# Kernel tuning notes

Measured on AMD Instinct MI355X. Metric: run time of the kernel, lower is better.

Reference implementation:

```python
import jax, jax.numpy as jnp
import numpy as np

TOPK = 8
MIN_TEMP = 0.5
NEG = -1e9  # finite stand-in for -inf (same softmax result, safe grads)


def setup_inputs() -> dict:
    key = jax.random.key(0)
    ks = jax.random.split(key, 6)
    B, S, D, N, K = 4, 4096, 1024, 256, 8
    token_states = jax.random.normal(ks[0], (B, S, D), dtype=jnp.float32)
    set_states = jax.random.normal(ks[1], (B, N, D), dtype=jnp.float32)
    desc_router = jax.random.normal(ks[2], (N, D), dtype=jnp.float32)
    token_to_sets = jax.random.randint(ks[3], (S, K), 0, N)
    Wq = jax.random.normal(ks[4], (D, D), dtype=jnp.float32) / np.sqrt(D)
    bq = jnp.zeros((D,), dtype=jnp.float32)
    temperature = jnp.ones((1,), dtype=jnp.float32)
    return {"token_states": token_states, "set_states": set_states,
            "desc_router": desc_router, "token_to_sets": token_to_sets,
            "Wq": Wq, "bq": bq, "temperature": temperature}


def reference(token_states, set_states, desc_router, token_to_sets, Wq, bq, temperature):
    B, S, D = token_states.shape
    N = set_states.shape[1]
    scale = 1.0 / np.sqrt(D)

    # q = Linear(token_states)
    q = jnp.einsum('bsd,ed->bse', token_states, Wq) + bq
    scores = jnp.einsum('bse,ne->bsn', q, desc_router) * scale  # [B,S,N]

    # restrict_to_sets: boolean routing mask built by scatter
    rows = jnp.broadcast_to(jnp.arange(S)[:, None], token_to_sets.shape)
    cols = jnp.clip(token_to_sets, 0, N - 1)
    valid = token_to_sets >= 0
    mask = jnp.zeros((S, N), dtype=bool).at[rows, cols].max(valid)
    scores = jnp.where(mask[None], scores, NEG)

    # top-k keep (topk < num_sets)
    topk_scores, topk_idx = jax.lax.top_k(scores, TOPK)
    b_idx = jnp.arange(B)[:, None, None]
    s_idx = jnp.arange(S)[None, :, None]
    keep = jnp.full_like(scores, NEG).at[b_idx, s_idx, topk_idx].set(topk_scores)

    temp = jnp.maximum(temperature, MIN_TEMP)  # clamp(min=0.5)
    weights = jax.nn.softmax(keep / temp, axis=-1)  # [B,S,N]
    token_repr = jnp.einsum('bsn,bnd->bsd', weights, set_states)
    bank_indices = jnp.argmax(weights, axis=-1)
    return token_repr, bank_indices, weights, topk_idx
```

## Files before the change

### kernel.cpp

```cpp
#include <hip/hip_runtime.h>
#include <math.h>
#include <float.h>


namespace {
constexpr int kB = 4, kS = 4096, kD = 1024, kN = 256, kK = 8;
constexpr float kScale = 0.03125f;
constexpr float kNeg = -1e9f;
constexpr float kLog2e = 1.4426950408889634f;
constexpr size_t kBankOff = (size_t)kB * kS * kD;
constexpr size_t kWOff    = kBankOff + (size_t)kB * kS;
constexpr size_t kTopkOff = kWOff + (size_t)kB * kS * kN;
constexpr int kEC = 8;
constexpr int kEL = kD / kEC;
constexpr int kNT = kN / 8;
}

#if __has_builtin(__builtin_amdgcn_exp2f)
#define FAST_EXP2(x) __builtin_amdgcn_exp2f(x)
#else
#define FAST_EXP2(x) exp2f(x)
#endif
#if __has_builtin(__builtin_amdgcn_rcpf)
#define FAST_RCP(x) __builtin_amdgcn_rcpf(x)
#else
#define FAST_RCP(x) (1.0f / (x))
#endif

__global__ __launch_bounds__(256) void k_prep(const float* __restrict__ dr,
                                              const float* __restrict__ wq,
                                              float* __restrict__ part) {
  const int nt = blockIdx.x, ec = blockIdx.y, t = threadIdx.x;
  const float4* wq4 = reinterpret_cast<const float4*>(wq);
  float4 acc[8];
#pragma unroll
  for (int j = 0; j < 8; ++j) acc[j] = make_float4(0.f, 0.f, 0.f, 0.f);
  const int e0 = ec * kEL;
#pragma unroll 4
  for (int e = e0; e < e0 + kEL; ++e) {
    const float4 wv = wq4[(size_t)e * (kD / 4) + t];
#pragma unroll
    for (int j = 0; j < 8; ++j) {
      const float a = dr[(size_t)(nt * 8 + j) * kD + e];
      acc[j].x += a * wv.x; acc[j].y += a * wv.y;
      acc[j].z += a * wv.z; acc[j].w += a * wv.w;
    }
  }
  float4* p4 = reinterpret_cast<float4*>(part);
#pragma unroll
  for (int j = 0; j < 8; ++j)
    p4[((size_t)ec * kN + nt * 8 + j) * (kD / 4) + t] = acc[j];
}

__global__ __launch_bounds__(256) void k_reduce(const float* __restrict__ part,
                                                const float* __restrict__ dr,
                                                const float* __restrict__ bq,
                                                float* __restrict__ R,
                                                float* __restrict__ bias) {
  const int n = blockIdx.x, t = threadIdx.x;
  const float4* p4 = reinterpret_cast<const float4*>(part);
  float4 a = make_float4(0.f, 0.f, 0.f, 0.f);
#pragma unroll
  for (int ec = 0; ec < kEC; ++ec) {
    const float4 p = p4[((size_t)ec * kN + n) * (kD / 4) + t];
    a.x += p.x; a.y += p.y; a.z += p.z; a.w += p.w;
  }
  a.x *= kScale; a.y *= kScale; a.z *= kScale; a.w *= kScale;
  reinterpret_cast<float4*>(R)[(size_t)n * (kD / 4) + t] = a;

  if (t < 64) {
    const float4* b4 = reinterpret_cast<const float4*>(bq);
    const float4* dr4 = reinterpret_cast<const float4*>(dr + (size_t)n * kD);
    float p = 0.f;
#pragma unroll
    for (int i = 0; i < 4; ++i) {
      const float4 bb = b4[t * 4 + i];
      const float4 dd = dr4[t * 4 + i];
      p += bb.x * dd.x + bb.y * dd.y + bb.z * dd.z + bb.w * dd.w;
    }
#pragma unroll
    for (int off = 32; off; off >>= 1) p += __shfl_xor(p, off);
    if (t == 0) bias[n] = p * kScale;
  }
}

__global__ __launch_bounds__(256, 4) void k_score(const float* __restrict__ ts,
                                                  const int* __restrict__ t2s,
                                                  const float* __restrict__ R,
                                                  const float* __restrict__ bias,
                                                  const float* __restrict__ temp_p,
                                                  int* __restrict__ st,
                                                  float* __restrict__ out) {
  const int lane = threadIdx.x & 63;
  const int wid = threadIdx.x >> 6;
  const int u = lane & 15;
  const int g = lane >> 4;
  const int s = __builtin_amdgcn_readfirstlane(blockIdx.x * 4 + wid);

  int nraw[kK], nk[kK];
#pragma unroll
  for (int k = 0; k < kK; ++k) {
    nraw[k] = t2s[s * kK + k];
    const int n = nraw[k];
    nk[k] = n < 0 ? 0 : (n > kN - 1 ? kN - 1 : n);
  }
  int validmask = 0;
#pragma unroll
  for (int k = 0; k < kK; ++k) {
    bool v = (nraw[k] >= 0);
#pragma unroll
    for (int j = 0; j < kK; ++j)
      if (j < k && nk[j] == nk[k]) v = false;
    validmask |= v ? (1 << k) : 0;
  }
  const int cnt = __popc(validmask);

  const float4* ts4 = reinterpret_cast<const float4*>(ts);
  const float4* R4 = reinterpret_cast<const float4*>(R);
  const size_t tbase = ((size_t)g * kS + s) * (kD / 4) + u;
  float acc[kK];
#pragma unroll
  for (int k = 0; k < kK; ++k) acc[k] = 0.f;
#pragma unroll 2
  for (int i = 0; i < 16; ++i) {
    const float4 tv = ts4[tbase + i * 16];
#pragma unroll
    for (int k = 0; k < kK; ++k) {
      const float4 rv = R4[(size_t)nk[k] * (kD / 4) + i * 16 + u];
      acc[k] += tv.x * rv.x + tv.y * rv.y + tv.z * rv.z + tv.w * rv.w;
    }
  }

  float pk[kK];
#pragma unroll
  for (int k = 0; k < kK; ++k) {
    float a = acc[k];
    a += __shfl_xor(a, 1);
    a += __shfl_xor(a, 2);
    a += __shfl_xor(a, 4);
    a += __shfl_xor(a, 8);
    pk[k] = a + bias[nk[k]];
  }

  unsigned long long pm0 = 0, pm1 = 0, pm2 = 0, pm3 = 0;
#pragma unroll
  for (int k = 0; k < kK; ++k) {
    const bool v = (validmask >> k) & 1;
    const unsigned long long bit = 1ull << (nk[k] & 63);
    const int wd = nk[k] >> 6;
    pm0 |= (v && wd == 0) ? bit : 0ull;
    pm1 |= (v && wd == 1) ? bit : 0ull;
    pm2 |= (v && wd == 2) ? bit : 0ull;
    pm3 |= (v && wd == 3) ? bit : 0ull;
  }
  int seq[kK];
#pragma unroll
  for (int i = 0; i < kK; ++i) {
    const unsigned long long i0 = ~pm0, i1 = ~pm1, i2 = ~pm2, i3 = ~pm3;
    const int c = i0 ? (__ffsll(i0) - 1)
                     : (i1 ? 64 + (__ffsll(i1) - 1)
                           : (i2 ? 128 + (__ffsll(i2) - 1)
                                 : 192 + (__ffsll(i3) - 1)));
    seq[i] = c;
    const unsigned long long b2 = 1ull << (c & 63);
    const int wd = c >> 6;
    pm0 |= (wd == 0) ? b2 : 0ull;
    pm1 |= (wd == 1) ? b2 : 0ull;
    pm2 |= (wd == 2) ? b2 : 0ull;
    pm3 |= (wd == 3) ? b2 : 0ull;
  }

  float fs[kK];
  int fi[kK];
#pragma unroll
  for (int k = 0; k < kK; ++k) {
    const bool v = (validmask >> k) & 1;
    const int jk = __popc((~validmask) & ((1 << k) - 1));
    int fv = seq[0];
#pragma unroll
    for (int j = 1; j < kK; ++j) fv = (jk == j) ? seq[j] : fv;
    fs[k] = v ? pk[k] : kNeg;
    fi[k] = v ? nk[k] : fv;
  }
#define CE(A, B)                                                        \
  {                                                                     \
    const bool sw = (fs[B] > fs[A]) || (fs[B] == fs[A] && fi[B] < fi[A]); \
    const float fa = fs[A], fb = fs[B];                                 \
    const int ia = fi[A], ib = fi[B];                                   \
    fs[A] = sw ? fb : fa; fs[B] = sw ? fa : fb;                         \
    fi[A] = sw ? ib : ia; fi[B] = sw ? ia : ib;                         \
  }
  CE(0,1) CE(2,3) CE(4,5) CE(6,7)
  CE(0,2) CE(1,3) CE(4,6) CE(5,7)
  CE(1,2) CE(5,6)
  CE(0,4) CE(1,5) CE(2,6) CE(3,7)
  CE(2,4) CE(3,5)
  CE(1,2) CE(3,4) CE(5,6)
#undef CE

  const float it = kLog2e * FAST_RCP(fmaxf(temp_p[0], 0.5f));
  float w[kK];
  float denom = 0.f;
#pragma unroll
  for (int i = 0; i < kK; ++i) {
    const float e = (i < cnt) ? FAST_EXP2((fs[i] - fs[0]) * it) : 0.f;
    w[i] = e;
    denom += e;
  }
  const float rd = FAST_RCP(denom);
#pragma unroll
  for (int i = 0; i < kK; ++i) w[i] *= rd;

  const size_t row = (size_t)g * kS + s;
  if (u < kK) {
    int v = fi[0];
#pragma unroll
    for (int k = 1; k < kK; ++k) v = (u == k) ? fi[k] : v;
    out[kTopkOff + row * kK + u] = (float)v;
  }
  if (u == 0) out[kBankOff + row] = (float)fi[0];

  int sel = 0;
#pragma unroll
  for (int k = 0; k < kK; ++k) {
    sel = (u == k) ? __float_as_int(w[k]) : sel;
    sel = (u == k + kK) ? fi[k] : sel;
  }
  st[row * 16 + u] = sel;
}

__global__ __launch_bounds__(256) void k_repr(const float* __restrict__ ss,
                                              const int* __restrict__ st,
                                              float* __restrict__ out) {
  const int lane = threadIdx.x & 63;
  const int wid = threadIdx.x >> 6;
  const int bid = blockIdx.x;
  const int xcd = bid & 7;
  const int b = xcd >> 1;
  int s_ = ((bid >> 3) << 2) + wid + ((xcd & 1) << 11);
  const int s = __builtin_amdgcn_readfirstlane(s_);
  const size_t row = (size_t)b * kS + s;

  float w[kK];
  int fi[kK];
#pragma unroll
  for (int k = 0; k < kK; ++k) {
    w[k] = __int_as_float(st[row * 16 + k]);
    fi[k] = st[row * 16 + kK + k];
  }

  const float4* ssb = reinterpret_cast<const float4*>(ss) + (size_t)b * kN * (kD / 4);
  float4* o4 = reinterpret_cast<float4*>(out) + row * (kD / 4);
#pragma unroll
  for (int c = 0; c < 4; ++c) {
    float4 v0 = ssb[(size_t)fi[0] * (kD / 4) + c * 64 + lane];
    float4 v1 = ssb[(size_t)fi[1] * (kD / 4) + c * 64 + lane];
    float4 v2 = ssb[(size_t)fi[2] * (kD / 4) + c * 64 + lane];
    float4 v3 = ssb[(size_t)fi[3] * (kD / 4) + c * 64 + lane];
    float4 v4 = ssb[(size_t)fi[4] * (kD / 4) + c * 64 + lane];
    float4 v5 = ssb[(size_t)fi[5] * (kD / 4) + c * 64 + lane];
    float4 v6 = ssb[(size_t)fi[6] * (kD / 4) + c * 64 + lane];
    float4 v7 = ssb[(size_t)fi[7] * (kD / 4) + c * 64 + lane];
    float4 acc;
    acc.x = w[0] * v0.x + w[1] * v1.x + w[2] * v2.x + w[3] * v3.x
          + w[4] * v4.x + w[5] * v5.x + w[6] * v6.x + w[7] * v7.x;
    acc.y = w[0] * v0.y + w[1] * v1.y + w[2] * v2.y + w[3] * v3.y
          + w[4] * v4.y + w[5] * v5.y + w[6] * v6.y + w[7] * v7.y;
    acc.z = w[0] * v0.z + w[1] * v1.z + w[2] * v2.z + w[3] * v3.z
          + w[4] * v4.z + w[5] * v5.z + w[6] * v6.z + w[7] * v7.z;
    acc.w = w[0] * v0.w + w[1] * v1.w + w[2] * v2.w + w[3] * v3.w
          + w[4] * v4.w + w[5] * v5.w + w[6] * v6.w + w[7] * v7.w;
    o4[c * 64 + lane] = acc;
  }

  {
    const int cb = lane * 4;
    float4 wv = make_float4(0.f, 0.f, 0.f, 0.f);
#pragma unroll
    for (int k = 0; k < kK; ++k) {
      wv.x = (fi[k] == cb    ) ? w[k] : wv.x;
      wv.y = (fi[k] == cb + 1) ? w[k] : wv.y;
      wv.z = (fi[k] == cb + 2) ? w[k] : wv.z;
      wv.w = (fi[k] == cb + 3) ? w[k] : wv.w;
    }
    reinterpret_cast<float4*>(out + kWOff)[row * (kN / 4) + lane] = wv;
  }
}

extern "C" void kernel_launch(void* const* d_in, const int* in_sizes, int n_in,
                              void* d_out, int out_size, void* d_ws, size_t ws_size,
                              hipStream_t stream) {
  const float* ts  = (const float*)d_in[0];
  const float* ss  = (const float*)d_in[1];
  const float* dr  = (const float*)d_in[2];
  const int*   t2s = (const int*)  d_in[3];
  const float* wq  = (const float*)d_in[4];
  const float* bq  = (const float*)d_in[5];
  const float* tmp = (const float*)d_in[6];
  float* out = (float*)d_out;

  float* R    = (float*)d_ws;
  float* bias = R + (size_t)kN * kD;
  int*   st   = (int*)(bias + kN);
  float* part = out + kWOff;

  k_prep<<<dim3(kNT, kEC), 256, 0, stream>>>(dr, wq, part);
  k_reduce<<<kN, 256, 0, stream>>>(part, dr, bq, R, bias);
  k_score<<<kS / 4, 256, 0, stream>>>(ts, t2s, R, bias, tmp, st, out);
  k_repr<<<kB * kS / 4, 256, 0, stream>>>(ss, st, out);
}
```

Measured before the change: 77.80 us.

## Restructure score kernel so each lane covers all batches, reusing each R row load

The score kernel now runs one 64-lane block per token. Each lane loads that token's states for all four batches into registers, then streams each routed R row once and dots it against all four batches, software-prefetching the next row. This removes the 16-lane split per batch, where each R row was reloaded per batch group, and replaces it with a transpose-style cross-group shuffle reduction. The trade-offs are much higher register use from holding 16 float4 values plus prefetch buffers, and four times as many small single-wave blocks.

New measurement: 72.09 us. -7.3%, faster.

```diff
diff --git a/kernel.cpp b/kernel.cpp
--- a/kernel.cpp
+++ b/kernel.cpp
@@ -84,18 +84,17 @@
   }
 }
 
-__global__ __launch_bounds__(256, 4) void k_score(const float* __restrict__ ts,
-                                                  const int* __restrict__ t2s,
-                                                  const float* __restrict__ R,
-                                                  const float* __restrict__ bias,
-                                                  const float* __restrict__ temp_p,
-                                                  int* __restrict__ st,
-                                                  float* __restrict__ out) {
-  const int lane = threadIdx.x & 63;
-  const int wid = threadIdx.x >> 6;
+__global__ __launch_bounds__(64, 3) void k_score(const float* __restrict__ ts,
+                                                 const int* __restrict__ t2s,
+                                                 const float* __restrict__ R,
+                                                 const float* __restrict__ bias,
+                                                 const float* __restrict__ temp_p,
+                                                 int* __restrict__ st,
+                                                 float* __restrict__ out) {
+  const int lane = threadIdx.x;
   const int u = lane & 15;
   const int g = lane >> 4;
-  const int s = __builtin_amdgcn_readfirstlane(blockIdx.x * 4 + wid);
+  const int s = blockIdx.x;
 
   int nraw[kK], nk[kK];
 #pragma unroll
@@ -117,29 +116,67 @@
 
   const float4* ts4 = reinterpret_cast<const float4*>(ts);
   const float4* R4 = reinterpret_cast<const float4*>(R);
-  const size_t tbase = ((size_t)g * kS + s) * (kD / 4) + u;
-  float acc[kK];
-#pragma unroll
-  for (int k = 0; k < kK; ++k) acc[k] = 0.f;
-#pragma unroll 2
-  for (int i = 0; i < 16; ++i) {
-    const float4 tv = ts4[tbase + i * 16];
+  float4 tv[kB][4];
+#pragma unroll
+  for (int t = 0; t < kB; ++t)
+#pragma unroll
+    for (int j = 0; j < 4; ++j)
+      tv[t][j] = ts4[((size_t)t * kS + s) * (kD / 4) + j * 64 + lane];
+
+  float acc[kB][kK];
+  float4 rc[4];
+#pragma unroll
+  for (int j = 0; j < 4; ++j)
+    rc[j] = R4[(size_t)nk[0] * (kD / 4) + j * 64 + lane];
+#pragma unroll
+  for (int k = 0; k < kK; ++k) {
+    float4 rn[4];
+    if (k + 1 < kK) {
+#pragma unroll
+      for (int j = 0; j < 4; ++j)
+        rn[j] = R4[(size_t)nk[k + 1] * (kD / 4) + j * 64 + lane];
+    }
+#pragma unroll
+    for (int t = 0; t < kB; ++t) {
+      float a = tv[t][0].x * rc[0].x + tv[t][0].y * rc[0].y
+              + tv[t][0].z * rc[0].z + tv[t][0].w * rc[0].w;
+      a += tv[t][1].x * rc[1].x + tv[t][1].y * rc[1].y
+         + tv[t][1].z * rc[1].z + tv[t][1].w * rc[1].w;
+      a += tv[t][2].x * rc[2].x + tv[t][2].y * rc[2].y
+         + tv[t][2].z * rc[2].z + tv[t][2].w * rc[2].w;
+      a += tv[t][3].x * rc[3].x + tv[t][3].y * rc[3].y
+         + tv[t][3].z * rc[3].z + tv[t][3].w * rc[3].w;
+      acc[t][k] = a;
+    }
+    if (k + 1 < kK) {
+#pragma unroll
+      for (int j = 0; j < 4; ++j) rc[j] = rn[j];
+    }
+  }
+
+#pragma unroll
+  for (int t = 0; t < kB; ++t)
 #pragma unroll
     for (int k = 0; k < kK; ++k) {
-      const float4 rv = R4[(size_t)nk[k] * (kD / 4) + i * 16 + u];
-      acc[k] += tv.x * rv.x + tv.y * rv.y + tv.z * rv.z + tv.w * rv.w;
-    }
-  }
+      float a = acc[t][k];
+      a += __shfl_xor(a, 1);
+      a += __shfl_xor(a, 2);
+      a += __shfl_xor(a, 4);
+      a += __shfl_xor(a, 8);
+      acc[t][k] = a;
+    }
 
   float pk[kK];
 #pragma unroll
   for (int k = 0; k < kK; ++k) {
-    float a = acc[k];
-    a += __shfl_xor(a, 1);
-    a += __shfl_xor(a, 2);
-    a += __shfl_xor(a, 4);
-    a += __shfl_xor(a, 8);
-    pk[k] = a + bias[nk[k]];
+    const float a0 = acc[0][k], a1 = acc[1][k], a2 = acc[2][k], a3 = acc[3][k];
+    float own = a0; own = (g == 1) ? a1 : own; own = (g == 2) ? a2 : own; own = (g == 3) ? a3 : own;
+    float x1  = a1; x1  = (g == 1) ? a0 : x1;  x1  = (g == 2) ? a3 : x1;  x1  = (g == 3) ? a2 : x1;
+    float x2  = a2; x2  = (g == 1) ? a3 : x2;  x2  = (g == 2) ? a0 : x2;  x2  = (g == 3) ? a1 : x2;
+    float x3  = a3; x3  = (g == 1) ? a2 : x3;  x3  = (g == 2) ? a1 : x3;  x3  = (g == 3) ? a0 : x3;
+    const float y = own + __shfl_xor(x1, 16);
+    const float z = x2 + __shfl_xor(x3, 16);
+    pk[k] = y + __shfl_xor(z, 32) + bias[nk[k]];
   }
 
   unsigned long long pm0 = 0, pm1 = 0, pm2 = 0, pm3 = 0;
@@ -306,6 +343,6 @@
 
   k_prep<<<dim3(kNT, kEC), 256, 0, stream>>>(dr, wq, part);
   k_reduce<<<kN, 256, 0, stream>>>(part, dr, bq, R, bias);
-  k_score<<<kS / 4, 256, 0, stream>>>(ts, t2s, R, bias, tmp, st, out);
+  k_score<<<kS, 64, 0, stream>>>(ts, t2s, R, bias, tmp, st, out);
   k_repr<<<kB * kS / 4, 256, 0, stream>>>(ss, st, out);
 }
```

## Score one token per block with cross-wave LDS reduction over the full D

Applied to the files above, without the earlier changes.

The score kernel now processes one sequence position per 256-thread block instead of four. Each thread loads one float4 from each of the four batch rows and the eight routed R rows, so the load is spread over the whole block rather than looped 16 times inside one wave. Partial dot products are reduced with a full 64-lane shuffle, then combined across the four waves through shared memory, with each wave then handling one batch row. This trades a longer per-wave loop for more blocks and more parallel memory requests, at the cost of a __syncthreads and more shuffle work, and it drops the occupancy hint from the launch bounds.

New measurement: 90.19 us. 15.9% more time.

```diff
diff --git a/kernel.cpp b/kernel.cpp
--- a/kernel.cpp
+++ b/kernel.cpp
@@ -84,18 +84,19 @@
   }
 }
 
-__global__ __launch_bounds__(256, 4) void k_score(const float* __restrict__ ts,
-                                                  const int* __restrict__ t2s,
-                                                  const float* __restrict__ R,
-                                                  const float* __restrict__ bias,
-                                                  const float* __restrict__ temp_p,
-                                                  int* __restrict__ st,
-                                                  float* __restrict__ out) {
-  const int lane = threadIdx.x & 63;
-  const int wid = threadIdx.x >> 6;
-  const int u = lane & 15;
-  const int g = lane >> 4;
-  const int s = __builtin_amdgcn_readfirstlane(blockIdx.x * 4 + wid);
+__global__ __launch_bounds__(256) void k_score(const float* __restrict__ ts,
+                                               const int* __restrict__ t2s,
+                                               const float* __restrict__ R,
+                                               const float* __restrict__ bias,
+                                               const float* __restrict__ temp_p,
+                                               int* __restrict__ st,
+                                               float* __restrict__ out) {
+  const int t = threadIdx.x;
+  const int lane = t & 63;
+  const int w = t >> 6;
+  const int s = blockIdx.x;
+
+  __shared__ float red[32 * 4];
 
   int nraw[kK], nk[kK];
 #pragma unroll
@@ -117,29 +118,59 @@
 
   const float4* ts4 = reinterpret_cast<const float4*>(ts);
   const float4* R4 = reinterpret_cast<const float4*>(R);
-  const size_t tbase = ((size_t)g * kS + s) * (kD / 4) + u;
-  float acc[kK];
-#pragma unroll
-  for (int k = 0; k < kK; ++k) acc[k] = 0.f;
-#pragma unroll 2
-  for (int i = 0; i < 16; ++i) {
-    const float4 tv = ts4[tbase + i * 16];
+  const int base = s * (kD / 4) + t;
+  const float4 a0 = ts4[base];
+  const float4 a1 = ts4[kS * (kD / 4) + base];
+  const float4 a2 = ts4[2 * kS * (kD / 4) + base];
+  const float4 a3 = ts4[3 * kS * (kD / 4) + base];
+  float4 rv[kK];
+#pragma unroll
+  for (int k = 0; k < kK; ++k) rv[k] = R4[nk[k] * (kD / 4) + t];
+  float bk[kK];
+#pragma unroll
+  for (int k = 0; k < kK; ++k) bk[k] = bias[nk[k]];
+  const float tmp0 = temp_p[0];
+
+  float p[kB][kK];
+#pragma unroll
+  for (int k = 0; k < kK; ++k) {
+    const float4 r = rv[k];
+    p[0][k] = a0.x * r.x + a0.y * r.y + a0.z * r.z + a0.w * r.w;
+    p[1][k] = a1.x * r.x + a1.y * r.y + a1.z * r.z + a1.w * r.w;
+    p[2][k] = a2.x * r.x + a2.y * r.y + a2.z * r.z + a2.w * r.w;
+    p[3][k] = a3.x * r.x + a3.y * r.y + a3.z * r.z + a3.w * r.w;
+  }
+
+#pragma unroll
+  for (int b = 0; b < kB; ++b)
 #pragma unroll
     for (int k = 0; k < kK; ++k) {
-      const float4 rv = R4[(size_t)nk[k] * (kD / 4) + i * 16 + u];
-      acc[k] += tv.x * rv.x + tv.y * rv.y + tv.z * rv.z + tv.w * rv.w;
+      float x = p[b][k];
+      x += __shfl_xor(x, 1);
+      x += __shfl_xor(x, 2);
+      x += __shfl_xor(x, 4);
+      x += __shfl_xor(x, 8);
+      x += __shfl_xor(x, 16);
+      x += __shfl_xor(x, 32);
+      p[b][k] = x;
     }
-  }
+
+  {
+    float v = p[0][0];
+#pragma unroll
+    for (int b = 0; b < kB; ++b)
+#pragma unroll
+      for (int k = 0; k < kK; ++k)
+        v = (lane == b * kK + k) ? p[b][k] : v;
+    if (lane < 32) red[lane * 4 + w] = v;
+  }
+  __syncthreads();
 
   float pk[kK];
 #pragma unroll
   for (int k = 0; k < kK; ++k) {
-    float a = acc[k];
-    a += __shfl_xor(a, 1);
-    a += __shfl_xor(a, 2);
-    a += __shfl_xor(a, 4);
-    a += __shfl_xor(a, 8);
-    pk[k] = a + bias[nk[k]];
+    const float4 q = *reinterpret_cast<const float4*>(&red[(w * kK + k) * 4]);
+    pk[k] = (q.x + q.y) + (q.z + q.w) + bk[k];
   }
 
   unsigned long long pm0 = 0, pm1 = 0, pm2 = 0, pm3 = 0;
@@ -198,35 +229,35 @@
   CE(1,2) CE(3,4) CE(5,6)
 #undef CE
 
-  const float it = kLog2e * FAST_RCP(fmaxf(temp_p[0], 0.5f));
-  float w[kK];
+  const float it = kLog2e * FAST_RCP(fmaxf(tmp0, 0.5f));
+  float wgt[kK];
   float denom = 0.f;
 #pragma unroll
   for (int i = 0; i < kK; ++i) {
     const float e = (i < cnt) ? FAST_EXP2((fs[i] - fs[0]) * it) : 0.f;
-    w[i] = e;
+    wgt[i] = e;
     denom += e;
   }
   const float rd = FAST_RCP(denom);
 #pragma unroll
-  for (int i = 0; i < kK; ++i) w[i] *= rd;
-
-  const size_t row = (size_t)g * kS + s;
-  if (u < kK) {
+  for (int i = 0; i < kK; ++i) wgt[i] *= rd;
+
+  const size_t row = (size_t)w * kS + s;
+  if (lane < kK) {
     int v = fi[0];
 #pragma unroll
-    for (int k = 1; k < kK; ++k) v = (u == k) ? fi[k] : v;
-    out[kTopkOff + row * kK + u] = (float)v;
-  }
-  if (u == 0) out[kBankOff + row] = (float)fi[0];
+    for (int k = 1; k < kK; ++k) v = (lane == k) ? fi[k] : v;
+    out[kTopkOff + row * kK + lane] = (float)v;
+  }
+  if (lane == 0) out[kBankOff + row] = (float)fi[0];
 
   int sel = 0;
 #pragma unroll
   for (int k = 0; k < kK; ++k) {
-    sel = (u == k) ? __float_as_int(w[k]) : sel;
-    sel = (u == k + kK) ? fi[k] : sel;
-  }
-  st[row * 16 + u] = sel;
+    sel = (lane == k) ? __float_as_int(wgt[k]) : sel;
+    sel = (lane == k + kK) ? fi[k] : sel;
+  }
+  if (lane < 16) st[row * 16 + lane] = sel;
 }
 
 __global__ __launch_bounds__(256) void k_repr(const float* __restrict__ ss,
@@ -306,6 +337,6 @@
 
   k_prep<<<dim3(kNT, kEC), 256, 0, stream>>>(dr, wq, part);
   k_reduce<<<kN, 256, 0, stream>>>(part, dr, bq, R, bias);
-  k_score<<<kS / 4, 256, 0, stream>>>(ts, t2s, R, bias, tmp, st, out);
+  k_score<<<kS, 256, 0, stream>>>(ts, t2s, R, bias, tmp, st, out);
   k_repr<<<kB * kS / 4, 256, 0, stream>>>(ss, st, out);
 }
```
